# Kernel optimization log

Measured on AMD Instinct MI355X. Metric: run time of the kernel, lower is better.

The kernel has to match this reference:

```python
import jax, jax.numpy as jnp
import numpy as np

N_NODES = 200000
F = 256
B = 8192
FAN1 = 16  # hop-1 fanout (layer_num_samples[0])
FAN2 = 4   # hop-2 fanout (layer_num_samples[1])


def setup_inputs() -> dict:
    key = jax.random.key(0)
    k1, k2, k3, k4, k5, k6 = jax.random.split(key, 6)
    node_feats = jax.random.normal(k1, (N_NODES, F), dtype=jnp.float32)
    # SageLayer weight: [out_size, 2*layer_size]
    W1 = jax.random.normal(k2, (F, 2 * F), dtype=jnp.float32) * 0.05
    W2 = jax.random.normal(k3, (F, 2 * F), dtype=jnp.float32) * 0.05
    batch_nodes = jax.random.randint(k4, (B,), 0, N_NODES)
    neigh1 = jax.random.randint(k5, (B, FAN1), 0, N_NODES)
    M1 = B + B * FAN1  # layer-1 node set: batch nodes + their sampled neighbors
    neigh2 = jax.random.randint(k6, (M1, FAN2), 0, N_NODES)
    return {"node_feats": node_feats, "W1": W1, "W2": W2,
            "batch_nodes": batch_nodes, "neigh1": neigh1, "neigh2": neigh2}


def reference(node_feats, W1, W2, batch_nodes, neigh1, neigh2):
    b = batch_nodes.shape[0]
    # layer-1 node list: batch nodes first, then hop-1 neighbors (row-major)
    nodes1 = jnp.concatenate([batch_nodes, neigh1.reshape(-1)])  # [17B]
    # ---- SAGE layer 1: MEAN-aggregate hop-2 neighbor raw features ----
    agg1 = node_feats[neigh2].mean(axis=1)              # [17B, F]
    self1 = node_feats[nodes1]                           # [17B, F]
    h1 = jax.nn.relu(jnp.concatenate([self1, agg1], axis=1) @ W1.T)  # [17B, F]
    # ---- SAGE layer 2: MEAN-aggregate hop-1 neighbors' hidden embs ----
    agg2 = h1[b:].reshape(b, neigh1.shape[1], -1).mean(axis=1)  # [B, F]
    h_self = h1[:b]                                      # [B, F]
    out = jax.nn.relu(jnp.concatenate([h_self, agg2], axis=1) @ W2.T)  # [B, F]
    return out
```

## Files before the change

kernel.cpp:

```cpp
#include <hip/hip_runtime.h>
#include <hip/hip_bf16.h>

#define NB 8192
#define M1T 139264
#define SELFB 128

typedef __attribute__((ext_vector_type(8))) short bf16x8;
typedef __attribute__((ext_vector_type(16))) float f32x16;

__device__ __forceinline__ unsigned short f2b(float f) {
  union { float f; unsigned u; } v; v.f = f;
  unsigned r = v.u + 0x7fffu + ((v.u >> 16) & 1u);
  return (unsigned short)(r >> 16);
}
__device__ __forceinline__ uint4 pack8u(float a0, float a1, float a2, float a3,
                                        float a4, float a5, float a6, float a7) {
  uint4 v;
  v.x = (unsigned)f2b(a0) | ((unsigned)f2b(a1) << 16);
  v.y = (unsigned)f2b(a2) | ((unsigned)f2b(a3) << 16);
  v.z = (unsigned)f2b(a4) | ((unsigned)f2b(a5) << 16);
  v.w = (unsigned)f2b(a6) | ((unsigned)f2b(a7) << 16);
  return v;
}

#define GLDS16(g, l)                                                          \
  __builtin_amdgcn_global_load_lds(                                           \
      (const __attribute__((address_space(1))) unsigned int*)(const void*)(g),\
      (__attribute__((address_space(3))) unsigned int*)(void*)(l), 16, 0, 0)

__global__ void convert_w(const float* __restrict__ W1, const float* __restrict__ W2,
                          unsigned short* __restrict__ W1s, unsigned short* __restrict__ W2s) {
  int i = blockIdx.x * 256 + threadIdx.x;
  const float* W; unsigned short* out; int f4;
  if (i < 32768) { W = W1; out = W1s; f4 = i; }
  else           { W = W2; out = W2s; f4 = i - 32768; }
  int n  = (f4 * 4) >> 9;
  int c0 = (f4 * 4) & 511;
  int kt = c0 >> 6;
  int slot = (c0 & 63) >> 3;
  int e  = c0 & 7;
  int sw = slot ^ (n & 7);
  float4 v = *((const float4*)W + f4);
  ushort4 o;
  o.x = f2b(v.x); o.y = f2b(v.y); o.z = f2b(v.z); o.w = f2b(v.w);
  *(ushort4*)(out + kt * 16384 + n * 64 + sw * 8 + e) = o;
}

__global__ __launch_bounds__(512, 4)
void sage_l1(const float* __restrict__ feats,
             const unsigned short* __restrict__ Wbs,
             const int* __restrict__ batch_nodes,
             const int* __restrict__ neigh1,
             const int* __restrict__ neigh2,
             unsigned short* __restrict__ A2)
{
  __shared__ __align__(16) unsigned short As[2][64 * 64];
  __shared__ __align__(16) unsigned short Bs[2][256 * 64];
  const int tid = threadIdx.x;
  const int m0 = blockIdx.x * 64;
  const int w = tid >> 6, lane = tid & 63, l31 = lane & 31, lh = lane >> 5;
  const int mh = w & 1, nq = w >> 1;
  const int m = tid >> 3, slot = tid & 7;
  const int r = m0 + m;

  const int self = (r < NB) ? batch_nodes[r] : neigh1[r - NB];
  const int4 nb = *(const int4*)(neigh2 + (size_t)r * 4);
  const char* fb = (const char*)feats;
  const unsigned so  = (unsigned)self * 1024u + (unsigned)slot * 32u;
  const unsigned no0 = (unsigned)nb.x * 1024u + (unsigned)slot * 32u;
  const unsigned no1 = (unsigned)nb.y * 1024u + (unsigned)slot * 32u;
  const unsigned no2 = (unsigned)nb.z * 1024u + (unsigned)slot * 32u;
  const unsigned no3 = (unsigned)nb.w * 1024u + (unsigned)slot * 32u;
  const int arowC = mh * 32 + l31;
  const int n0C = nq * 64 + l31, n1C = n0C + 32;

  f32x16 acc0 = {}, acc1 = {};
  float4 a0[8], a1[8];

  #define L1_LOADS(KT, AR)                                                    \
    do { if ((KT) < 4) {                                                      \
           AR[0] = *(const float4*)(fb + so + (KT) * 256);                    \
           AR[1] = *(const float4*)(fb + so + (KT) * 256 + 16);               \
         } else {                                                             \
           const int _kb = ((KT) - 4) * 256;                                  \
           AR[0] = *(const float4*)(fb + no0 + _kb);                          \
           AR[1] = *(const float4*)(fb + no0 + _kb + 16);                     \
           AR[2] = *(const float4*)(fb + no1 + _kb);                          \
           AR[3] = *(const float4*)(fb + no1 + _kb + 16);                     \
           AR[4] = *(const float4*)(fb + no2 + _kb);                          \
           AR[5] = *(const float4*)(fb + no2 + _kb + 16);                     \
           AR[6] = *(const float4*)(fb + no3 + _kb);                          \
           AR[7] = *(const float4*)(fb + no3 + _kb + 16);                     \
         } } while (0)

  #define L1_BISSUE(KT)                                                       \
    do { const unsigned short* _s = Wbs + (size_t)(KT) * 16384;               \
         unsigned short* _d = &Bs[(KT) & 1][0];                               \
         _Pragma("unroll")                                                    \
         for (int _q = 0; _q < 4; ++_q) {                                     \
           int _i = _q * 512 + tid;                                           \
           GLDS16(_s + (size_t)_i * 8, _d + _i * 8);                          \
         } } while (0)

  #define L1_CONV(KT, AR, AV)                                                 \
    do { if ((KT) < 4) {                                                      \
           AV = pack8u(AR[0].x, AR[0].y, AR[0].z, AR[0].w,                    \
                       AR[1].x, AR[1].y, AR[1].z, AR[1].w);                   \
         } else {                                                             \
           float s0 = AR[0].x + AR[2].x + AR[4].x + AR[6].x;                  \
           float s1 = AR[0].y + AR[2].y + AR[4].y + AR[6].y;                  \
           float s2 = AR[0].z + AR[2].z + AR[4].z + AR[6].z;                  \
           float s3 = AR[0].w + AR[2].w + AR[4].w + AR[6].w;                  \
           float s4 = AR[1].x + AR[3].x + AR[5].x + AR[7].x;                  \
           float s5 = AR[1].y + AR[3].y + AR[5].y + AR[7].y;                  \
           float s6 = AR[1].z + AR[3].z + AR[5].z + AR[7].z;                  \
           float s7 = AR[1].w + AR[3].w + AR[5].w + AR[7].w;                  \
           AV = pack8u(s0 * 0.25f, s1 * 0.25f, s2 * 0.25f, s3 * 0.25f,       \
                       s4 * 0.25f, s5 * 0.25f, s6 * 0.25f, s7 * 0.25f);      \
         } } while (0)

  #define L1_STEP(KT, AR, NCNT)                                               \
    do { uint4 _av;                                                           \
         L1_CONV(KT, AR, _av);      \
         *(uint4*)(&As[(KT) & 1][m * 64 + ((slot ^ (m & 7)) << 3)]) = _av;    \
         asm volatile("s_waitcnt vmcnt(" #NCNT ") lgkmcnt(0)" ::: "memory");  \
         __builtin_amdgcn_s_barrier();                                        \
         if ((KT) < 7) L1_BISSUE((KT) + 1);                                   \
         if ((KT) < 6) L1_LOADS((KT) + 2, AR);                                \
         __builtin_amdgcn_sched_barrier(0);                                   \
         __builtin_amdgcn_s_setprio(1);                                       \
         _Pragma("unroll")                                                    \
         for (int _kk = 0; _kk < 4; ++_kk) {                                  \
           int _sl = _kk * 2 + lh;                                            \
           bf16x8 _a  = *(const bf16x8*)(&As[(KT) & 1][arowC * 64 + ((_sl ^ (arowC & 7)) << 3)]); \
           bf16x8 _b0 = *(const bf16x8*)(&Bs[(KT) & 1][n0C * 64 + ((_sl ^ (n0C & 7)) << 3)]);     \
           bf16x8 _b1 = *(const bf16x8*)(&Bs[(KT) & 1][n1C * 64 + ((_sl ^ (n1C & 7)) << 3)]);     \
           acc0 = __builtin_amdgcn_mfma_f32_32x32x16_bf16(_a, _b0, acc0, 0, 0, 0);                \
           acc1 = __builtin_amdgcn_mfma_f32_32x32x16_bf16(_a, _b1, acc1, 0, 0, 0);                \
         }                                                                    \
         __builtin_amdgcn_s_setprio(0);                                       \
    } while (0)

  L1_LOADS(0, a0);
  L1_BISSUE(0);
  L1_LOADS(1, a1);
  __builtin_amdgcn_sched_barrier(0);

  L1_STEP(0, a0, 2);
  L1_STEP(1, a1, 2);
  L1_STEP(2, a0, 2);
  L1_STEP(3, a1, 8);
  L1_STEP(4, a0, 8);
  L1_STEP(5, a1, 8);
  L1_STEP(6, a0, 8);
  L1_STEP(7, a1, 0);

  #undef L1_LOADS
  #undef L1_BISSUE
  #undef L1_CONV
  #undef L1_STEP

  if (blockIdx.x < SELFB) {
    #pragma unroll
    for (int q = 0; q < 16; ++q) {
      int row = m0 + mh * 32 + (q & 3) + 8 * (q >> 2) + 4 * lh;
      int col0 = nq * 64 + l31;
      float v0 = acc0[q], v1 = acc1[q];
      v0 = v0 > 0.f ? v0 : 0.f;
      v1 = v1 > 0.f ? v1 : 0.f;
      A2[(size_t)row * 512 + col0] = f2b(v0);
      A2[(size_t)row * 512 + col0 + 32] = f2b(v1);
    }
  } else {
    const int bi = blockIdx.x - SELFB;
    #pragma unroll
    for (int gi = 0; gi < 2; ++gi) {
      float sA = 0.f, sB = 0.f;
      #pragma unroll
      for (int q = gi * 8; q < gi * 8 + 8; ++q) {
        float v0 = acc0[q], v1 = acc1[q];
        sA += (v0 > 0.f ? v0 : 0.f);
        sB += (v1 > 0.f ? v1 : 0.f);
      }
      sA += __shfl_xor(sA, 32, 64);
      sB += __shfl_xor(sB, 32, 64);
      if (lh == 0) {
        int gr = bi * 4 + mh * 2 + gi;
        int col = 256 + nq * 64 + l31;
        A2[(size_t)gr * 512 + col] = f2b(sA * 0.0625f);
        A2[(size_t)gr * 512 + col + 32] = f2b(sB * 0.0625f);
      }
    }
  }
}

__global__ __launch_bounds__(256, 2)
void sage_l2(const unsigned short* __restrict__ A2,
             const unsigned short* __restrict__ Wbs,
             float* __restrict__ out)
{
  __shared__ __align__(16) unsigned short As[2][32 * 64];
  __shared__ __align__(16) unsigned short Bs[2][256 * 64];
  const int tid = threadIdx.x;
  const int m0 = blockIdx.x * 32;
  const int w = tid >> 6, lane = tid & 63, l31 = lane & 31, lh = lane >> 5;
  const int mA = tid >> 3, swA = tid & 7;
  const int arowC = l31;
  const int n0C = w * 64 + l31, n1C = n0C + 32;
  const unsigned short* aSrc = A2 + (size_t)(m0 + mA) * 512 + (swA ^ (mA & 7)) * 8;

  f32x16 acc0 = {}, acc1 = {};

  #define L2_STAGE(KT)                                                        \
    do { const unsigned short* _s = Wbs + (size_t)(KT) * 16384;               \
         unsigned short* _d = &Bs[(KT) & 1][0];                               \
         _Pragma("unroll")                                                    \
         for (int _q = 0; _q < 8; ++_q) {                                     \
           int _i = _q * 256 + tid;                                           \
           GLDS16(_s + (size_t)_i * 8, _d + _i * 8);                          \
         }                                                                    \
         GLDS16(aSrc + (KT) * 64, &As[(KT) & 1][mA * 64 + swA * 8]);          \
    } while (0)

  L2_STAGE(0);
  asm volatile("s_waitcnt vmcnt(0)" ::: "memory");
  __builtin_amdgcn_s_barrier();

  #pragma unroll
  for (int kt = 0; kt < 8; ++kt) {
    if (kt < 7) L2_STAGE(kt + 1);
    __builtin_amdgcn_s_setprio(1);
    #pragma unroll
    for (int kk = 0; kk < 4; ++kk) {
      int sl = kk * 2 + lh;
      bf16x8 a  = *(const bf16x8*)(&As[kt & 1][arowC * 64 + ((sl ^ (arowC & 7)) << 3)]);
      bf16x8 b0 = *(const bf16x8*)(&Bs[kt & 1][n0C * 64 + ((sl ^ (n0C & 7)) << 3)]);
      bf16x8 b1 = *(const bf16x8*)(&Bs[kt & 1][n1C * 64 + ((sl ^ (n1C & 7)) << 3)]);
      acc0 = __builtin_amdgcn_mfma_f32_32x32x16_bf16(a, b0, acc0, 0, 0, 0);
      acc1 = __builtin_amdgcn_mfma_f32_32x32x16_bf16(a, b1, acc1, 0, 0, 0);
    }
    __builtin_amdgcn_s_setprio(0);
    asm volatile("s_waitcnt vmcnt(0)" ::: "memory");
    __builtin_amdgcn_s_barrier();
  }
  #undef L2_STAGE

  #pragma unroll
  for (int q = 0; q < 16; ++q) {
    int row = m0 + (q & 3) + 8 * (q >> 2) + 4 * lh;
    float v0 = acc0[q], v1 = acc1[q];
    out[(size_t)row * 256 + n0C] = v0 > 0.f ? v0 : 0.f;
    out[(size_t)row * 256 + n1C] = v1 > 0.f ? v1 : 0.f;
  }
}

extern "C" void kernel_launch(void* const* d_in, const int* in_sizes, int n_in,
                              void* d_out, int out_size, void* d_ws, size_t ws_size,
                              hipStream_t stream) {
  const float* feats       = (const float*)d_in[0];
  const float* W1          = (const float*)d_in[1];
  const float* W2          = (const float*)d_in[2];
  const int*   batch_nodes = (const int*)d_in[3];
  const int*   neigh1      = (const int*)d_in[4];
  const int*   neigh2      = (const int*)d_in[5];
  float* out = (float*)d_out;

  unsigned short* W1s = (unsigned short*)d_ws;
  unsigned short* W2s = W1s + 131072;
  unsigned short* A2  = W2s + 131072;

  hipLaunchKernelGGL(convert_w, dim3(256), dim3(256), 0, stream, W1, W2, W1s, W2s);
  hipLaunchKernelGGL(sage_l1, dim3(M1T / 64), dim3(512), 0, stream,
                     feats, W1s, batch_nodes, neigh1, neigh2, A2);
  hipLaunchKernelGGL(sage_l2, dim3(NB / 32), dim3(256), 0, stream, A2, W2s, out);
}
```

Measured before the change: 126.9 us.

## Pre-convert node feature table to bf16 and gather half-width rows

```diff
diff --git a/kernel.cpp b/kernel.cpp
--- a/kernel.cpp
+++ b/kernel.cpp
@@ -4,14 +4,20 @@
 #define NB 8192
 #define M1T 139264
 #define SELFB 128
+#define NFEAT 51200000
 
 typedef __attribute__((ext_vector_type(8))) short bf16x8;
 typedef __attribute__((ext_vector_type(16))) float f32x16;
+typedef __attribute__((ext_vector_type(4))) float f32x4;
 
 __device__ __forceinline__ unsigned short f2b(float f) {
   union { float f; unsigned u; } v; v.f = f;
   unsigned r = v.u + 0x7fffu + ((v.u >> 16) & 1u);
   return (unsigned short)(r >> 16);
+}
+__device__ __forceinline__ float b2f(unsigned u16) {
+  union { unsigned u; float f; } v; v.u = u16 << 16;
+  return v.f;
 }
 __device__ __forceinline__ uint4 pack8u(float a0, float a1, float a2, float a3,
                                         float a4, float a5, float a6, float a7) {
@@ -40,19 +46,30 @@
   int slot = (c0 & 63) >> 3;
   int e  = c0 & 7;
   int sw = slot ^ (n & 7);
-  float4 v = *((const float4*)W + f4);
+  f32x4 v = *((const f32x4*)W + f4);
   ushort4 o;
-  o.x = f2b(v.x); o.y = f2b(v.y); o.z = f2b(v.z); o.w = f2b(v.w);
+  o.x = f2b(v[0]); o.y = f2b(v[1]); o.z = f2b(v[2]); o.w = f2b(v[3]);
   *(ushort4*)(out + kt * 16384 + n * 64 + sw * 8 + e) = o;
 }
 
+__global__ __launch_bounds__(256)
+void conv_feats(const float* __restrict__ feats, unsigned short* __restrict__ featsb) {
+  const int stride = gridDim.x * 256;
+  for (size_t s = (size_t)blockIdx.x * 256 + threadIdx.x; s < NFEAT / 8; s += stride) {
+    const f32x4* p = (const f32x4*)feats + s * 2;
+    f32x4 x = __builtin_nontemporal_load(p);
+    f32x4 y = __builtin_nontemporal_load(p + 1);
+    *((uint4*)featsb + s) = pack8u(x[0], x[1], x[2], x[3], y[0], y[1], y[2], y[3]);
+  }
+}
+
 __global__ __launch_bounds__(512, 4)
-void sage_l1(const float* __restrict__ feats,
-             const unsigned short* __restrict__ Wbs,
-             const int* __restrict__ batch_nodes,
-             const int* __restrict__ neigh1,
-             const int* __restrict__ neigh2,
-             unsigned short* __restrict__ A2)
+void sage_l1_bf(const unsigned short* __restrict__ featsb,
+                const unsigned short* __restrict__ Wbs,
+                const int* __restrict__ batch_nodes,
+                const int* __restrict__ neigh1,
+                const int* __restrict__ neigh2,
+                unsigned short* __restrict__ A2)
 {
   __shared__ __align__(16) unsigned short As[2][64 * 64];
   __shared__ __align__(16) unsigned short Bs[2][256 * 64];
@@ -65,32 +82,27 @@
 
   const int self = (r < NB) ? batch_nodes[r] : neigh1[r - NB];
   const int4 nb = *(const int4*)(neigh2 + (size_t)r * 4);
-  const char* fb = (const char*)feats;
-  const unsigned so  = (unsigned)self * 1024u + (unsigned)slot * 32u;
-  const unsigned no0 = (unsigned)nb.x * 1024u + (unsigned)slot * 32u;
-  const unsigned no1 = (unsigned)nb.y * 1024u + (unsigned)slot * 32u;
-  const unsigned no2 = (unsigned)nb.z * 1024u + (unsigned)slot * 32u;
-  const unsigned no3 = (unsigned)nb.w * 1024u + (unsigned)slot * 32u;
+  const char* fb = (const char*)featsb;
+  const unsigned so  = (unsigned)self * 512u + (unsigned)slot * 16u;
+  const unsigned no0 = (unsigned)nb.x * 512u + (unsigned)slot * 16u;
+  const unsigned no1 = (unsigned)nb.y * 512u + (unsigned)slot * 16u;
+  const unsigned no2 = (unsigned)nb.z * 512u + (unsigned)slot * 16u;
+  const unsigned no3 = (unsigned)nb.w * 512u + (unsigned)slot * 16u;
   const int arowC = mh * 32 + l31;
   const int n0C = nq * 64 + l31, n1C = n0C + 32;
 
   f32x16 acc0 = {}, acc1 = {};
-  float4 a0[8], a1[8];
+  uint4 a0[4], a1[4];
 
   #define L1_LOADS(KT, AR)                                                    \
     do { if ((KT) < 4) {                                                      \
-           AR[0] = *(const float4*)(fb + so + (KT) * 256);                    \
-           AR[1] = *(const float4*)(fb + so + (KT) * 256 + 16);               \
+           AR[0] = *(const uint4*)(fb + so + (KT) * 128);                     \
          } else {                                                             \
-           const int _kb = ((KT) - 4) * 256;                                  \
-           AR[0] = *(const float4*)(fb + no0 + _kb);                          \
-           AR[1] = *(const float4*)(fb + no0 + _kb + 16);                     \
-           AR[2] = *(const float4*)(fb + no1 + _kb);                          \
-           AR[3] = *(const float4*)(fb + no1 + _kb + 16);                     \
-           AR[4] = *(const float4*)(fb + no2 + _kb);                          \
-           AR[5] = *(const float4*)(fb + no2 + _kb + 16);                     \
-           AR[6] = *(const float4*)(fb + no3 + _kb);                          \
-           AR[7] = *(const float4*)(fb + no3 + _kb + 16);                     \
+           const int _kb = ((KT) - 4) * 128;                                  \
+           AR[0] = *(const uint4*)(fb + no0 + _kb);                           \
+           AR[1] = *(const uint4*)(fb + no1 + _kb);                           \
+           AR[2] = *(const uint4*)(fb + no2 + _kb);                           \
+           AR[3] = *(const uint4*)(fb + no3 + _kb);                           \
          } } while (0)
 
   #define L1_BISSUE(KT)                                                       \
@@ -103,20 +115,18 @@
          } } while (0)
 
   #define L1_CONV(KT, AR, AV)                                                 \
-    do { if ((KT) < 4) {                                                      \
-           AV = pack8u(AR[0].x, AR[0].y, AR[0].z, AR[0].w,                    \
-                       AR[1].x, AR[1].y, AR[1].z, AR[1].w);                   \
-         } else {                                                             \
-           float s0 = AR[0].x + AR[2].x + AR[4].x + AR[6].x;                  \
-           float s1 = AR[0].y + AR[2].y + AR[4].y + AR[6].y;                  \
-           float s2 = AR[0].z + AR[2].z + AR[4].z + AR[6].z;                  \
-           float s3 = AR[0].w + AR[2].w + AR[4].w + AR[6].w;                  \
-           float s4 = AR[1].x + AR[3].x + AR[5].x + AR[7].x;                  \
-           float s5 = AR[1].y + AR[3].y + AR[5].y + AR[7].y;                  \
-           float s6 = AR[1].z + AR[3].z + AR[5].z + AR[7].z;                  \
-           float s7 = AR[1].w + AR[3].w + AR[5].w + AR[7].w;                  \
-           AV = pack8u(s0 * 0.25f, s1 * 0.25f, s2 * 0.25f, s3 * 0.25f,       \
-                       s4 * 0.25f, s5 * 0.25f, s6 * 0.25f, s7 * 0.25f);      \
+    do { if ((KT) < 4) { AV = AR[0]; }                                        \
+         else {                                                               \
+           float s0 = 0, s1 = 0, s2 = 0, s3 = 0, s4 = 0, s5 = 0, s6 = 0, s7 = 0; \
+           _Pragma("unroll")                                                  \
+           for (int _j = 0; _j < 4; ++_j) {                                   \
+             s0 += b2f(AR[_j].x & 0xffffu); s1 += b2f(AR[_j].x >> 16);        \
+             s2 += b2f(AR[_j].y & 0xffffu); s3 += b2f(AR[_j].y >> 16);        \
+             s4 += b2f(AR[_j].z & 0xffffu); s5 += b2f(AR[_j].z >> 16);        \
+             s6 += b2f(AR[_j].w & 0xffffu); s7 += b2f(AR[_j].w >> 16);        \
+           }                                                                  \
+           AV = pack8u(s0 * 0.25f, s1 * 0.25f, s2 * 0.25f, s3 * 0.25f,        \
+                       s4 * 0.25f, s5 * 0.25f, s6 * 0.25f, s7 * 0.25f);       \
          } } while (0)
 
   #define L1_STEP(KT, AR, NCNT)                                               \
@@ -146,13 +156,13 @@
   L1_LOADS(1, a1);
   __builtin_amdgcn_sched_barrier(0);
 
-  L1_STEP(0, a0, 2);
-  L1_STEP(1, a1, 2);
-  L1_STEP(2, a0, 2);
-  L1_STEP(3, a1, 8);
-  L1_STEP(4, a0, 8);
-  L1_STEP(5, a1, 8);
-  L1_STEP(6, a0, 8);
+  L1_STEP(0, a0, 1);
+  L1_STEP(1, a1, 1);
+  L1_STEP(2, a0, 1);
+  L1_STEP(3, a1, 4);
+  L1_STEP(4, a0, 4);
+  L1_STEP(5, a1, 4);
+  L1_STEP(6, a0, 4);
   L1_STEP(7, a1, 0);
 
   #undef L1_LOADS
@@ -194,6 +204,154 @@
   }
 }
 
+__global__ __launch_bounds__(512, 4)
+void sage_l1_f32(const float* __restrict__ feats,
+                 const unsigned short* __restrict__ Wbs,
+                 const int* __restrict__ batch_nodes,
+                 const int* __restrict__ neigh1,
+                 const int* __restrict__ neigh2,
+                 unsigned short* __restrict__ A2)
+{
+  __shared__ __align__(16) unsigned short As[2][64 * 64];
+  __shared__ __align__(16) unsigned short Bs[2][256 * 64];
+  const int tid = threadIdx.x;
+  const int m0 = blockIdx.x * 64;
+  const int w = tid >> 6, lane = tid & 63, l31 = lane & 31, lh = lane >> 5;
+  const int mh = w & 1, nq = w >> 1;
+  const int m = tid >> 3, slot = tid & 7;
+  const int r = m0 + m;
+
+  const int self = (r < NB) ? batch_nodes[r] : neigh1[r - NB];
+  const int4 nb = *(const int4*)(neigh2 + (size_t)r * 4);
+  const char* fb = (const char*)feats;
+  const unsigned so  = (unsigned)self * 1024u + (unsigned)slot * 32u;
+  const unsigned no0 = (unsigned)nb.x * 1024u + (unsigned)slot * 32u;
+  const unsigned no1 = (unsigned)nb.y * 1024u + (unsigned)slot * 32u;
+  const unsigned no2 = (unsigned)nb.z * 1024u + (unsigned)slot * 32u;
+  const unsigned no3 = (unsigned)nb.w * 1024u + (unsigned)slot * 32u;
+  const int arowC = mh * 32 + l31;
+  const int n0C = nq * 64 + l31, n1C = n0C + 32;
+
+  f32x16 acc0 = {}, acc1 = {};
+  f32x4 a0[8], a1[8];
+
+  #define L1F_LOADS(KT, AR)                                                   \
+    do { if ((KT) < 4) {                                                      \
+           AR[0] = *(const f32x4*)(fb + so + (KT) * 256);                     \
+           AR[1] = *(const f32x4*)(fb + so + (KT) * 256 + 16);                \
+         } else {                                                             \
+           const int _kb = ((KT) - 4) * 256;                                  \
+           AR[0] = *(const f32x4*)(fb + no0 + _kb);                           \
+           AR[1] = *(const f32x4*)(fb + no0 + _kb + 16);                      \
+           AR[2] = *(const f32x4*)(fb + no1 + _kb);                           \
+           AR[3] = *(const f32x4*)(fb + no1 + _kb + 16);                      \
+           AR[4] = *(const f32x4*)(fb + no2 + _kb);                           \
+           AR[5] = *(const f32x4*)(fb + no2 + _kb + 16);                      \
+           AR[6] = *(const f32x4*)(fb + no3 + _kb);                           \
+           AR[7] = *(const f32x4*)(fb + no3 + _kb + 16);                      \
+         } } while (0)
+
+  #define L1F_BISSUE(KT)                                                      \
+    do { const unsigned short* _s = Wbs + (size_t)(KT) * 16384;               \
+         unsigned short* _d = &Bs[(KT) & 1][0];                               \
+         _Pragma("unroll")                                                    \
+         for (int _q = 0; _q < 4; ++_q) {                                     \
+           int _i = _q * 512 + tid;                                           \
+           GLDS16(_s + (size_t)_i * 8, _d + _i * 8);                          \
+         } } while (0)
+
+  #define L1F_CONV(KT, AR, AV)                                                \
+    do { if ((KT) < 4) {                                                      \
+           AV = pack8u(AR[0][0], AR[0][1], AR[0][2], AR[0][3],                \
+                       AR[1][0], AR[1][1], AR[1][2], AR[1][3]);               \
+         } else {                                                             \
+           float s0 = AR[0][0] + AR[2][0] + AR[4][0] + AR[6][0];              \
+           float s1 = AR[0][1] + AR[2][1] + AR[4][1] + AR[6][1];              \
+           float s2 = AR[0][2] + AR[2][2] + AR[4][2] + AR[6][2];              \
+           float s3 = AR[0][3] + AR[2][3] + AR[4][3] + AR[6][3];              \
+           float s4 = AR[1][0] + AR[3][0] + AR[5][0] + AR[7][0];              \
+           float s5 = AR[1][1] + AR[3][1] + AR[5][1] + AR[7][1];              \
+           float s6 = AR[1][2] + AR[3][2] + AR[5][2] + AR[7][2];              \
+           float s7 = AR[1][3] + AR[3][3] + AR[5][3] + AR[7][3];              \
+           AV = pack8u(s0 * 0.25f, s1 * 0.25f, s2 * 0.25f, s3 * 0.25f,        \
+                       s4 * 0.25f, s5 * 0.25f, s6 * 0.25f, s7 * 0.25f);       \
+         } } while (0)
+
+  #define L1F_STEP(KT, AR, NCNT)                                              \
+    do { uint4 _av;                                                           \
+         L1F_CONV(KT, AR, _av);                                               \
+         *(uint4*)(&As[(KT) & 1][m * 64 + ((slot ^ (m & 7)) << 3)]) = _av;    \
+         asm volatile("s_waitcnt vmcnt(" #NCNT ") lgkmcnt(0)" ::: "memory");  \
+         __builtin_amdgcn_s_barrier();                                        \
+         if ((KT) < 7) L1F_BISSUE((KT) + 1);                                  \
+         if ((KT) < 6) L1F_LOADS((KT) + 2, AR);                               \
+         __builtin_amdgcn_sched_barrier(0);                                   \
+         __builtin_amdgcn_s_setprio(1);                                       \
+         _Pragma("unroll")                                                    \
+         for (int _kk = 0; _kk < 4; ++_kk) {                                  \
+           int _sl = _kk * 2 + lh;                                            \
+           bf16x8 _a  = *(const bf16x8*)(&As[(KT) & 1][arowC * 64 + ((_sl ^ (arowC & 7)) << 3)]); \
+           bf16x8 _b0 = *(const bf16x8*)(&Bs[(KT) & 1][n0C * 64 + ((_sl ^ (n0C & 7)) << 3)]);     \
+           bf16x8 _b1 = *(const bf16x8*)(&Bs[(KT) & 1][n1C * 64 + ((_sl ^ (n1C & 7)) << 3)]);     \
+           acc0 = __builtin_amdgcn_mfma_f32_32x32x16_bf16(_a, _b0, acc0, 0, 0, 0);                \
+           acc1 = __builtin_amdgcn_mfma_f32_32x32x16_bf16(_a, _b1, acc1, 0, 0, 0);                \
+         }                                                                    \
+         __builtin_amdgcn_s_setprio(0);                                       \
+    } while (0)
+
+  L1F_LOADS(0, a0);
+  L1F_BISSUE(0);
+  L1F_LOADS(1, a1);
+  __builtin_amdgcn_sched_barrier(0);
+
+  L1F_STEP(0, a0, 2);
+  L1F_STEP(1, a1, 2);
+  L1F_STEP(2, a0, 2);
+  L1F_STEP(3, a1, 8);
+  L1F_STEP(4, a0, 8);
+  L1F_STEP(5, a1, 8);
+  L1F_STEP(6, a0, 8);
+  L1F_STEP(7, a1, 0);
+
+  #undef L1F_LOADS
+  #undef L1F_BISSUE
+  #undef L1F_CONV
+  #undef L1F_STEP
+
+  if (blockIdx.x < SELFB) {
+    #pragma unroll
+    for (int q = 0; q < 16; ++q) {
+      int row = m0 + mh * 32 + (q & 3) + 8 * (q >> 2) + 4 * lh;
+      int col0 = nq * 64 + l31;
+      float v0 = acc0[q], v1 = acc1[q];
+      v0 = v0 > 0.f ? v0 : 0.f;
+      v1 = v1 > 0.f ? v1 : 0.f;
+      A2[(size_t)row * 512 + col0] = f2b(v0);
+      A2[(size_t)row * 512 + col0 + 32] = f2b(v1);
+    }
+  } else {
+    const int bi = blockIdx.x - SELFB;
+    #pragma unroll
+    for (int gi = 0; gi < 2; ++gi) {
+      float sA = 0.f, sB = 0.f;
+      #pragma unroll
+      for (int q = gi * 8; q < gi * 8 + 8; ++q) {
+        float v0 = acc0[q], v1 = acc1[q];
+        sA += (v0 > 0.f ? v0 : 0.f);
+        sB += (v1 > 0.f ? v1 : 0.f);
+      }
+      sA += __shfl_xor(sA, 32, 64);
+      sB += __shfl_xor(sB, 32, 64);
+      if (lh == 0) {
+        int gr = bi * 4 + mh * 2 + gi;
+        int col = 256 + nq * 64 + l31;
+        A2[(size_t)gr * 512 + col] = f2b(sA * 0.0625f);
+        A2[(size_t)gr * 512 + col + 32] = f2b(sB * 0.0625f);
+      }
+    }
+  }
+}
+
 __global__ __launch_bounds__(256, 2)
 void sage_l2(const unsigned short* __restrict__ A2,
              const unsigned short* __restrict__ Wbs,
@@ -265,12 +423,21 @@
   const int*   neigh2      = (const int*)d_in[5];
   float* out = (float*)d_out;
 
-  unsigned short* W1s = (unsigned short*)d_ws;
-  unsigned short* W2s = W1s + 131072;
-  unsigned short* A2  = W2s + 131072;
+  unsigned short* W1s   = (unsigned short*)d_ws;
+  unsigned short* W2s   = W1s + 131072;
+  unsigned short* A2    = W2s + 131072;
+  unsigned short* featsb = A2 + (size_t)NB * 512;
+
+  const size_t need = ((size_t)131072 * 2 + (size_t)NB * 512 + (size_t)NFEAT) * 2;
 
   hipLaunchKernelGGL(convert_w, dim3(256), dim3(256), 0, stream, W1, W2, W1s, W2s);
-  hipLaunchKernelGGL(sage_l1, dim3(M1T / 64), dim3(512), 0, stream,
-                     feats, W1s, batch_nodes, neigh1, neigh2, A2);
+  if (ws_size >= need) {
+    hipLaunchKernelGGL(conv_feats, dim3(3200), dim3(256), 0, stream, feats, featsb);
+    hipLaunchKernelGGL(sage_l1_bf, dim3(M1T / 64), dim3(512), 0, stream,
+                       featsb, W1s, batch_nodes, neigh1, neigh2, A2);
+  } else {
+    hipLaunchKernelGGL(sage_l1_f32, dim3(M1T / 64), dim3(512), 0, stream,
+                       feats, W1s, batch_nodes, neigh1, neigh2, A2);
+  }
   hipLaunchKernelGGL(sage_l2, dim3(NB / 32), dim3(256), 0, stream, A2, W2s, out);
 }
```

Result: slower. 141.6 us (+11.6%).
